# Kernel optimization log

Hardware: AMD Instinct MI355X
Metric: run time of the kernel (lower is better)

Reference implementation:

```python
import jax, jax.numpy as jnp
import numpy as np

DIM, HEADS, WH, WW, MLAT, MLON = 512, 8, 8, 8, 32, 64
N = WH * WW
B = MLAT * MLON
PER_LAT = (2 * WH - 1) * (2 * WW - 1)  # 225


def _make_rel_idx():
    # Swin 2D relative position index inside one window
    ch, cw = np.arange(WH), np.arange(WW)
    coords = np.stack(np.meshgrid(ch, cw, indexing='ij')).reshape(2, -1)  # (2, N)
    rel = coords[:, :, None] - coords[:, None, :]                          # (2, N, N)
    rel = rel.transpose(1, 2, 0).astype(np.int64)
    rel[..., 0] += WH - 1
    rel[..., 1] += WW - 1
    rel[..., 0] *= 2 * WW - 1
    idx2d = rel.sum(-1)                                                    # (N, N)
    # earth-specific: each lat row i gets its own 225-entry slab; lon diff is 0
    idx = idx2d[None] + np.arange(MLAT)[:, None, None] * PER_LAT           # (Mlat, N, N)
    idx = np.broadcast_to(idx[:, None], (MLAT, MLON, N, N)).reshape(B, N, N)
    return jnp.asarray(idx.astype(np.int32))


def setup_inputs() -> dict:
    key = jax.random.key(0)
    k = jax.random.split(key, 5)
    x = jax.random.normal(k[0], (B, N, DIM), dtype=jnp.float32)
    w_qkv = jax.random.normal(k[1], (3 * DIM, DIM), dtype=jnp.float32) * 0.02
    b_qkv = jnp.zeros((3 * DIM,), dtype=jnp.float32)
    w_proj = jax.random.normal(k[2], (DIM, DIM), dtype=jnp.float32) * 0.02
    b_proj = jnp.zeros((DIM,), dtype=jnp.float32)
    bias_table = jax.random.normal(k[3], (MLAT * PER_LAT, HEADS), dtype=jnp.float32) * 0.02
    return {
        'x': x, 'w_qkv': w_qkv, 'b_qkv': b_qkv,
        'w_proj': w_proj, 'b_proj': b_proj,
        'bias_table': bias_table, 'rel_idx': _make_rel_idx(),
    }


def reference(x, w_qkv, b_qkv, w_proj, b_proj, bias_table, rel_idx):
    Bn, Nn, C = x.shape
    D = C // HEADS
    qkv = (x @ w_qkv.T + b_qkv).reshape(Bn, Nn, 3, HEADS, D)
    q = jnp.transpose(qkv[:, :, 0], (0, 2, 1, 3))  # (B, H, N, D)
    k = jnp.transpose(qkv[:, :, 1], (0, 2, 1, 3))
    v = jnp.transpose(qkv[:, :, 2], (0, 2, 1, 3))
    # gather learned earth bias: (B, N, N, H) -> (B, H, N, N)
    bias = jnp.transpose(bias_table[rel_idx], (0, 3, 1, 2))
    scale = D ** -0.5  # SDPA default scale (qk_scale is None)
    attn = jax.nn.softmax(jnp.einsum('bhnd,bhmd->bhnm', q, k) * scale + bias, axis=-1)
    out = jnp.einsum('bhnm,bhmd->bhnd', attn, v)
    out = jnp.transpose(out, (0, 2, 1, 3)).reshape(Bn, Nn, C)
    return out @ w_proj.T + b_proj
```

## Files before the change

kernel.cpp:

```cpp
#include <hip/hip_runtime.h>
#include <stdint.h>

typedef __attribute__((ext_vector_type(8))) short short8;
typedef __attribute__((ext_vector_type(4))) short short4v;
typedef __attribute__((ext_vector_type(4))) float float4v;

__device__ __forceinline__ short f2bf(float f) {
  uint32_t u = __builtin_bit_cast(uint32_t, f);
  u += 0x7FFFu + ((u >> 16) & 1u);
  return (short)(u >> 16);
}

__device__ __forceinline__ void gl_lds16(const short* g, short* l) {
  __builtin_amdgcn_global_load_lds(
      (const __attribute__((address_space(1))) unsigned int*)g,
      (__attribute__((address_space(3))) unsigned int*)l, 16, 0, 0);
}

#define XPITCH 520
#define QPITCH 72

__global__ void prep_weights(const float* __restrict__ wq, const float* __restrict__ wp,
                             short* __restrict__ wq_b, short* __restrict__ wp_b) {
  int i = blockIdx.x * blockDim.x + threadIdx.x;
  int stride = gridDim.x * blockDim.x;
  for (int j = i; j < 786432 / 4; j += stride) {
    float4 v = ((const float4*)wq)[j];
    short4v t = {f2bf(v.x), f2bf(v.y), f2bf(v.z), f2bf(v.w)};
    ((short4v*)wq_b)[j] = t;
  }
  for (int j = i; j < 262144 / 4; j += stride) {
    float4 v = ((const float4*)wp)[j];
    short4v t = {f2bf(v.x), f2bf(v.y), f2bf(v.z), f2bf(v.w)};
    ((short4v*)wp_b)[j] = t;
  }
}

__global__ __launch_bounds__(512, 2)
void qkv_attn(const float* __restrict__ x, const short* __restrict__ wq,
              const float* __restrict__ bqkv, const float* __restrict__ btab,
              short* __restrict__ attn) {
  __shared__ short Xs[64 * XPITCH];
  __shared__ short Qs[2][64 * QPITCH];
  __shared__ short Ks[2][64 * QPITCH];
  __shared__ short Vt[2][64 * QPITCH];

  const int b    = blockIdx.x;
  const int tid  = threadIdx.x;
  const int lane = tid & 63;
  const int w    = tid >> 6;
  const int l16  = lane & 15;
  const int quad = lane >> 4;
  const int lat  = b >> 6;

  const float* xw = x + (size_t)b * (64 * 512);
  for (int c = tid; c < 64 * 128; c += 512) {
    int n = c >> 7, kc = c & 127;
    float4 v = *(const float4*)(xw + n * 512 + kc * 4);
    short4v t = {f2bf(v.x), f2bf(v.y), f2bf(v.z), f2bf(v.w)};
    *(short4v*)&Xs[n * XPITCH + kc * 4] = t;
  }
  __syncthreads();

  const int g  = w >> 2;
  const int st = w & 3;

  for (int h0 = 0; h0 < 8; h0 += 2) {
    {
      const int hq = h0 + g;
      const int hk = h0 + 1 - g;
      const short* Aq = wq + (size_t)((hq * 64 + st * 16 + l16) * 512) + quad * 8;
      const short* Ak = wq + (size_t)(((512) + hk * 64 + st * 16 + l16) * 512) + quad * 8;
      const short* Av = wq + (size_t)(((1024) + hq * 64 + st * 16 + l16) * 512) + quad * 8;
      const short* xb0 = &Xs[l16 * XPITCH + quad * 8];
      const short* xb1 = xb0 + 16 * XPITCH;
      const short* xb2 = xb0 + 32 * XPITCH;
      const short* xb3 = xb0 + 48 * XPITCH;

      float4v aQ[4] = {}, aK[4] = {}, aV[4] = {};
#pragma unroll 4
      for (int kk = 0; kk < 512; kk += 32) {
        short8 wqf = *(const short8*)(Aq + kk);
        short8 wkf = *(const short8*)(Ak + kk);
        short8 wvf = *(const short8*)(Av + kk);
        short8 x0 = *(const short8*)(xb0 + kk);
        short8 x1 = *(const short8*)(xb1 + kk);
        short8 x2 = *(const short8*)(xb2 + kk);
        short8 x3 = *(const short8*)(xb3 + kk);
        aQ[0] = __builtin_amdgcn_mfma_f32_16x16x32_bf16(wqf, x0, aQ[0], 0, 0, 0);
        aQ[1] = __builtin_amdgcn_mfma_f32_16x16x32_bf16(wqf, x1, aQ[1], 0, 0, 0);
        aQ[2] = __builtin_amdgcn_mfma_f32_16x16x32_bf16(wqf, x2, aQ[2], 0, 0, 0);
        aQ[3] = __builtin_amdgcn_mfma_f32_16x16x32_bf16(wqf, x3, aQ[3], 0, 0, 0);
        aK[0] = __builtin_amdgcn_mfma_f32_16x16x32_bf16(wkf, x0, aK[0], 0, 0, 0);
        aK[1] = __builtin_amdgcn_mfma_f32_16x16x32_bf16(wkf, x1, aK[1], 0, 0, 0);
        aK[2] = __builtin_amdgcn_mfma_f32_16x16x32_bf16(wkf, x2, aK[2], 0, 0, 0);
        aK[3] = __builtin_amdgcn_mfma_f32_16x16x32_bf16(wkf, x3, aK[3], 0, 0, 0);
        aV[0] = __builtin_amdgcn_mfma_f32_16x16x32_bf16(x0, wvf, aV[0], 0, 0, 0);
        aV[1] = __builtin_amdgcn_mfma_f32_16x16x32_bf16(x1, wvf, aV[1], 0, 0, 0);
        aV[2] = __builtin_amdgcn_mfma_f32_16x16x32_bf16(x2, wvf, aV[2], 0, 0, 0);
        aV[3] = __builtin_amdgcn_mfma_f32_16x16x32_bf16(x3, wvf, aV[3], 0, 0, 0);
      }

      float bq[4], bk[4];
#pragma unroll
      for (int i = 0; i < 4; ++i) {
        bq[i] = bqkv[hq * 64 + st * 16 + quad * 4 + i];
        bk[i] = bqkv[512 + hk * 64 + st * 16 + quad * 4 + i];
      }
      short* dq = &Qs[g][0];
      short* dk = &Ks[1 - g][0];
#pragma unroll
      for (int t = 0; t < 4; ++t) {
        int n = t * 16 + l16;
        short4v pq, pk;
#pragma unroll
        for (int i = 0; i < 4; ++i) {
          pq[i] = f2bf((aQ[t][i] + bq[i]) * 0.125f);
          pk[i] = f2bf(aK[t][i] + bk[i]);
        }
        *(short4v*)&dq[n * QPITCH + st * 16 + quad * 4] = pq;
        *(short4v*)&dk[n * QPITCH + st * 16 + quad * 4] = pk;
      }
      float bv = bqkv[1024 + hq * 64 + st * 16 + l16];
#pragma unroll
      for (int t = 0; t < 4; ++t) {
        short4v pv;
#pragma unroll
        for (int i = 0; i < 4; ++i) pv[i] = f2bf(aV[t][i] + bv);
        *(short4v*)&Vt[g][(st * 16 + l16) * QPITCH + t * 16 + quad * 4] = pv;
      }
    }
    __syncthreads();

    {
      const int hsel = w >> 2;
      const int h    = h0 + hsel;
      const int n0   = (w & 3) * 16;

      float4v s4[4] = {};
#pragma unroll
      for (int kd = 0; kd < 64; kd += 32) {
        short8 a = *(const short8*)&Qs[hsel][(n0 + l16) * QPITCH + kd + quad * 8];
#pragma unroll
        for (int t = 0; t < 4; ++t) {
          short8 bf = *(const short8*)&Ks[hsel][(t * 16 + l16) * QPITCH + kd + quad * 8];
          s4[t] = __builtin_amdgcn_mfma_f32_16x16x32_bf16(a, bf, s4[t], 0, 0, 0);
        }
      }
#pragma unroll
      for (int t = 0; t < 4; ++t) {
        int m = t * 16 + l16;
#pragma unroll
        for (int i = 0; i < 4; ++i) {
          int n = n0 + quad * 4 + i;
          int idx = ((n >> 3) - (m >> 3) + 7) * 15 + ((n & 7) - (m & 7) + 7) + lat * 225;
          s4[t][i] += btab[idx * 8 + h];
        }
      }
      float p[4][4];
#pragma unroll
      for (int i = 0; i < 4; ++i) {
        float mx = fmaxf(fmaxf(s4[0][i], s4[1][i]), fmaxf(s4[2][i], s4[3][i]));
        mx = fmaxf(mx, __shfl_xor(mx, 1));
        mx = fmaxf(mx, __shfl_xor(mx, 2));
        mx = fmaxf(mx, __shfl_xor(mx, 4));
        mx = fmaxf(mx, __shfl_xor(mx, 8));
        float e0 = __expf(s4[0][i] - mx), e1 = __expf(s4[1][i] - mx);
        float e2 = __expf(s4[2][i] - mx), e3 = __expf(s4[3][i] - mx);
        float sm = e0 + e1 + e2 + e3;
        sm += __shfl_xor(sm, 1);
        sm += __shfl_xor(sm, 2);
        sm += __shfl_xor(sm, 4);
        sm += __shfl_xor(sm, 8);
        float inv = 1.0f / sm;
        p[0][i] = e0 * inv; p[1][i] = e1 * inv; p[2][i] = e2 * inv; p[3][i] = e3 * inv;
      }
#pragma unroll
      for (int t = 0; t < 4; ++t)
#pragma unroll
        for (int i = 0; i < 4; ++i)
          Qs[hsel][(n0 + quad * 4 + i) * QPITCH + t * 16 + l16] = f2bf(p[t][i]);

      float4v o4[4] = {};
#pragma unroll
      for (int km = 0; km < 64; km += 32) {
        short8 a = *(const short8*)&Qs[hsel][(n0 + l16) * QPITCH + km + quad * 8];
#pragma unroll
        for (int t = 0; t < 4; ++t) {
          short8 bf = *(const short8*)&Vt[hsel][(t * 16 + l16) * QPITCH + km + quad * 8];
          o4[t] = __builtin_amdgcn_mfma_f32_16x16x32_bf16(a, bf, o4[t], 0, 0, 0);
        }
      }
      short* ob = attn + (size_t)b * (64 * 512);
#pragma unroll
      for (int t = 0; t < 4; ++t)
#pragma unroll
        for (int i = 0; i < 4; ++i)
          ob[(n0 + quad * 4 + i) * 512 + h * 64 + t * 16 + l16] = f2bf(o4[t][i]);
    }
    __syncthreads();
  }
}

__global__ __launch_bounds__(256, 2)
void proj_gemm(const short* __restrict__ attn, const short* __restrict__ wp,
               const float* __restrict__ bproj, float* __restrict__ out) {
  __shared__ short As[128 * 64];
  __shared__ short Bs[128 * 64];

  const int orig = blockIdx.x;
  const int wg   = (orig & 7) * 512 + (orig >> 3);
  const int n0   = (wg & 3) * 128;
  const int m0   = (wg >> 2) * 128;

  const int tid  = threadIdx.x;
  const int lane = tid & 63;
  const int w    = tid >> 6;
  const int l16  = lane & 15;
  const int quad = lane >> 4;
  const int wm   = w >> 1, wn = w & 1;

  const int srow = lane >> 3;
  const int scol = (lane & 7) * 8;

  float4v acc[4][4] = {};

  for (int kk = 0; kk < 512; kk += 64) {
#pragma unroll
    for (int j = 0; j < 4; ++j) {
      int chunk = w * 4 + j;
      int row = chunk * 8 + srow;
      gl_lds16(attn + (size_t)(m0 + row) * 512 + kk + scol, &As[chunk * 512]);
      gl_lds16(wp + (size_t)(n0 + row) * 512 + kk + scol, &Bs[chunk * 512]);
    }
    __syncthreads();
#pragma unroll
    for (int ks = 0; ks < 64; ks += 32) {
      short8 a[4], bf[4];
#pragma unroll
      for (int ti = 0; ti < 4; ++ti)
        a[ti] = *(const short8*)&As[(wm * 64 + ti * 16 + l16) * 64 + ks + quad * 8];
#pragma unroll
      for (int tj = 0; tj < 4; ++tj)
        bf[tj] = *(const short8*)&Bs[(wn * 64 + tj * 16 + l16) * 64 + ks + quad * 8];
#pragma unroll
      for (int ti = 0; ti < 4; ++ti)
#pragma unroll
        for (int tj = 0; tj < 4; ++tj)
          acc[ti][tj] = __builtin_amdgcn_mfma_f32_16x16x32_bf16(a[ti], bf[tj], acc[ti][tj], 0, 0, 0);
    }
    __syncthreads();
  }

  float bj[4];
#pragma unroll
  for (int tj = 0; tj < 4; ++tj) bj[tj] = bproj[n0 + wn * 64 + tj * 16 + l16];
#pragma unroll
  for (int ti = 0; ti < 4; ++ti)
#pragma unroll
    for (int i = 0; i < 4; ++i) {
      size_t rowoff = (size_t)(m0 + wm * 64 + ti * 16 + quad * 4 + i) * 512;
#pragma unroll
      for (int tj = 0; tj < 4; ++tj)
        out[rowoff + n0 + wn * 64 + tj * 16 + l16] = acc[ti][tj][i] + bj[tj];
    }
}

extern "C" void kernel_launch(void* const* d_in, const int* in_sizes, int n_in,
                              void* d_out, int out_size, void* d_ws, size_t ws_size,
                              hipStream_t stream) {
  const float* x     = (const float*)d_in[0];
  const float* wqkv  = (const float*)d_in[1];
  const float* bqkv  = (const float*)d_in[2];
  const float* wproj = (const float*)d_in[3];
  const float* bproj = (const float*)d_in[4];
  const float* btab  = (const float*)d_in[5];
  float* out = (float*)d_out;

  short* wq_b = (short*)d_ws;
  short* wp_b = wq_b + 786432;
  short* attn = wp_b + 262144;

  prep_weights<<<256, 256, 0, stream>>>(wqkv, wproj, wq_b, wp_b);
  qkv_attn<<<2048, 512, 0, stream>>>(x, wq_b, bqkv, btab, attn);
  proj_gemm<<<4096, 256, 0, stream>>>(attn, wp_b, bproj, out);
}
```

Baseline: 1.063 ms.

## Swizzle LDS layouts, process four heads per block, double-buffer projection GEMM

The padded LDS pitches are replaced by XOR-swizzled layouts for the X, Q, K, V and P tiles in the attention kernel and for the projection GEMM tiles. This is meant to avoid bank conflicts without wasting LDS on padding. The attention kernel now runs 1024 threads per block and handles four heads per pass instead of two, halving the number of head-loop iterations and barriers. The projection GEMM moves to 512 threads with smaller per-wave tiles and a two-stage LDS double buffer, so global-to-LDS loads overlap MFMA work. In exchange, LDS use per block grows to the full budget and register pressure is tighter under the new launch bounds.

```diff
diff --git a/kernel.cpp b/kernel.cpp
--- a/kernel.cpp
+++ b/kernel.cpp
@@ -17,8 +17,6 @@
       (__attribute__((address_space(3))) unsigned int*)l, 16, 0, 0);
 }
 
-#define XPITCH 520
-#define QPITCH 72
 
 __global__ void prep_weights(const float* __restrict__ wq, const float* __restrict__ wp,
                              short* __restrict__ wq_b, short* __restrict__ wp_b) {
@@ -36,14 +34,14 @@
   }
 }
 
-__global__ __launch_bounds__(512, 2)
+__global__ __launch_bounds__(1024, 4)
 void qkv_attn(const float* __restrict__ x, const short* __restrict__ wq,
               const float* __restrict__ bqkv, const float* __restrict__ btab,
               short* __restrict__ attn) {
-  __shared__ short Xs[64 * XPITCH];
-  __shared__ short Qs[2][64 * QPITCH];
-  __shared__ short Ks[2][64 * QPITCH];
-  __shared__ short Vt[2][64 * QPITCH];
+  __shared__ short Xs[64 * 512];
+  __shared__ short Qs[4][64 * 64];
+  __shared__ short Ks[4][64 * 64];
+  __shared__ short Vt[4][64 * 64];
 
   const int b    = blockIdx.x;
   const int tid  = threadIdx.x;
@@ -52,41 +50,45 @@
   const int l16  = lane & 15;
   const int quad = lane >> 4;
   const int lat  = b >> 6;
+  const int r    = l16 & 7;
+  const int offE = ((quad ^ (r & 3)) << 3) | ((r >> 2) << 5);
+  const int offO = offE ^ 32;
 
   const float* xw = x + (size_t)b * (64 * 512);
-  for (int c = tid; c < 64 * 128; c += 512) {
+  for (int c = tid; c < 64 * 128; c += 1024) {
     int n = c >> 7, kc = c & 127;
     float4 v = *(const float4*)(xw + n * 512 + kc * 4);
     short4v t = {f2bf(v.x), f2bf(v.y), f2bf(v.z), f2bf(v.w)};
-    *(short4v*)&Xs[n * XPITCH + kc * 4] = t;
+    *(short4v*)&Xs[n * 512 + ((kc * 4) ^ ((n & 7) << 3))] = t;
   }
   __syncthreads();
 
   const int g  = w >> 2;
   const int st = w & 3;
 
-  for (int h0 = 0; h0 < 8; h0 += 2) {
+#pragma unroll 1
+  for (int h0 = 0; h0 < 8; h0 += 4) {
     {
       const int hq = h0 + g;
-      const int hk = h0 + 1 - g;
+      const int hk = h0 + (g ^ 1);
       const short* Aq = wq + (size_t)((hq * 64 + st * 16 + l16) * 512) + quad * 8;
-      const short* Ak = wq + (size_t)(((512) + hk * 64 + st * 16 + l16) * 512) + quad * 8;
-      const short* Av = wq + (size_t)(((1024) + hq * 64 + st * 16 + l16) * 512) + quad * 8;
-      const short* xb0 = &Xs[l16 * XPITCH + quad * 8];
-      const short* xb1 = xb0 + 16 * XPITCH;
-      const short* xb2 = xb0 + 32 * XPITCH;
-      const short* xb3 = xb0 + 48 * XPITCH;
+      const short* Ak = wq + (size_t)((512 + hk * 64 + st * 16 + l16) * 512) + quad * 8;
+      const short* Av = wq + (size_t)((1024 + hq * 64 + st * 16 + l16) * 512) + quad * 8;
+      const short* xE = &Xs[l16 * 512 + offE];
+      const short* xO = &Xs[l16 * 512 + offO];
 
       float4v aQ[4] = {}, aK[4] = {}, aV[4] = {};
-#pragma unroll 4
-      for (int kk = 0; kk < 512; kk += 32) {
-        short8 wqf = *(const short8*)(Aq + kk);
-        short8 wkf = *(const short8*)(Ak + kk);
-        short8 wvf = *(const short8*)(Av + kk);
-        short8 x0 = *(const short8*)(xb0 + kk);
-        short8 x1 = *(const short8*)(xb1 + kk);
-        short8 x2 = *(const short8*)(xb2 + kk);
-        short8 x3 = *(const short8*)(xb3 + kk);
+#pragma unroll
+      for (int j = 0; j < 16; ++j) {
+        const short* xb = (j & 1) ? xO : xE;
+        const int xoff = (j >> 1) * 64;
+        short8 wqf = *(const short8*)(Aq + j * 32);
+        short8 wkf = *(const short8*)(Ak + j * 32);
+        short8 wvf = *(const short8*)(Av + j * 32);
+        short8 x0 = *(const short8*)(xb + xoff);
+        short8 x1 = *(const short8*)(xb + 8192 + xoff);
+        short8 x2 = *(const short8*)(xb + 16384 + xoff);
+        short8 x3 = *(const short8*)(xb + 24576 + xoff);
         aQ[0] = __builtin_amdgcn_mfma_f32_16x16x32_bf16(wqf, x0, aQ[0], 0, 0, 0);
         aQ[1] = __builtin_amdgcn_mfma_f32_16x16x32_bf16(wqf, x1, aQ[1], 0, 0, 0);
         aQ[2] = __builtin_amdgcn_mfma_f32_16x16x32_bf16(wqf, x2, aQ[2], 0, 0, 0);
@@ -108,7 +110,8 @@
         bk[i] = bqkv[512 + hk * 64 + st * 16 + quad * 4 + i];
       }
       short* dq = &Qs[g][0];
-      short* dk = &Ks[1 - g][0];
+      short* dk = &Ks[g ^ 1][0];
+      const int swqk = (st * 16 + quad * 4) ^ (r << 3);
 #pragma unroll
       for (int t = 0; t < 4; ++t) {
         int n = t * 16 + l16;
@@ -118,16 +121,17 @@
           pq[i] = f2bf((aQ[t][i] + bq[i]) * 0.125f);
           pk[i] = f2bf(aK[t][i] + bk[i]);
         }
-        *(short4v*)&dq[n * QPITCH + st * 16 + quad * 4] = pq;
-        *(short4v*)&dk[n * QPITCH + st * 16 + quad * 4] = pk;
+        *(short4v*)&dq[n * 64 + swqk] = pq;
+        *(short4v*)&dk[n * 64 + swqk] = pk;
       }
       float bv = bqkv[1024 + hq * 64 + st * 16 + l16];
+      const int dv = st * 16 + l16;
 #pragma unroll
       for (int t = 0; t < 4; ++t) {
         short4v pv;
 #pragma unroll
         for (int i = 0; i < 4; ++i) pv[i] = f2bf(aV[t][i] + bv);
-        *(short4v*)&Vt[g][(st * 16 + l16) * QPITCH + t * 16 + quad * 4] = pv;
+        *(short4v*)&Vt[g][dv * 64 + ((t * 16 + quad * 4) ^ (r << 3))] = pv;
       }
     }
     __syncthreads();
@@ -136,14 +140,18 @@
       const int hsel = w >> 2;
       const int h    = h0 + hsel;
       const int n0   = (w & 3) * 16;
+      const short* Qb = &Qs[hsel][0];
+      const short* Kb = &Ks[hsel][0];
+      const short* Vb = &Vt[hsel][0];
 
       float4v s4[4] = {};
 #pragma unroll
-      for (int kd = 0; kd < 64; kd += 32) {
-        short8 a = *(const short8*)&Qs[hsel][(n0 + l16) * QPITCH + kd + quad * 8];
+      for (int j = 0; j < 2; ++j) {
+        const int o = j ? offO : offE;
+        short8 a = *(const short8*)&Qb[(n0 + l16) * 64 + o];
 #pragma unroll
         for (int t = 0; t < 4; ++t) {
-          short8 bf = *(const short8*)&Ks[hsel][(t * 16 + l16) * QPITCH + kd + quad * 8];
+          short8 bf = *(const short8*)&Kb[(t * 16 + l16) * 64 + o];
           s4[t] = __builtin_amdgcn_mfma_f32_16x16x32_bf16(a, bf, s4[t], 0, 0, 0);
         }
       }
@@ -175,19 +183,23 @@
         float inv = 1.0f / sm;
         p[0][i] = e0 * inv; p[1][i] = e1 * inv; p[2][i] = e2 * inv; p[3][i] = e3 * inv;
       }
+      short* Pw = &Qs[hsel][0];
 #pragma unroll
       for (int t = 0; t < 4; ++t)
 #pragma unroll
-        for (int i = 0; i < 4; ++i)
-          Qs[hsel][(n0 + quad * 4 + i) * QPITCH + t * 16 + l16] = f2bf(p[t][i]);
+        for (int i = 0; i < 4; ++i) {
+          int row = n0 + quad * 4 + i;
+          Pw[row * 64 + ((t * 16 + l16) ^ ((row & 7) << 3))] = f2bf(p[t][i]);
+        }
 
       float4v o4[4] = {};
 #pragma unroll
-      for (int km = 0; km < 64; km += 32) {
-        short8 a = *(const short8*)&Qs[hsel][(n0 + l16) * QPITCH + km + quad * 8];
+      for (int j = 0; j < 2; ++j) {
+        const int o = j ? offO : offE;
+        short8 a = *(const short8*)&Qb[(n0 + l16) * 64 + o];
 #pragma unroll
         for (int t = 0; t < 4; ++t) {
-          short8 bf = *(const short8*)&Vt[hsel][(t * 16 + l16) * QPITCH + km + quad * 8];
+          short8 bf = *(const short8*)&Vb[(t * 16 + l16) * 64 + o];
           o4[t] = __builtin_amdgcn_mfma_f32_16x16x32_bf16(a, bf, o4[t], 0, 0, 0);
         }
       }
@@ -202,11 +214,47 @@
   }
 }
 
-__global__ __launch_bounds__(256, 2)
+__device__ __forceinline__ void stage_tile(const short* __restrict__ ga,
+                                           const short* __restrict__ gb,
+                                           short* lA, short* lB,
+                                           int w, int srow, int scol) {
+#pragma unroll
+  for (int j = 0; j < 2; ++j) {
+    int c = w * 2 + j;
+    gl_lds16(ga + (size_t)(c * 8 + srow) * 512 + scol, &lA[c * 512]);
+    gl_lds16(gb + (size_t)(c * 8 + srow) * 512 + scol, &lB[c * 512]);
+  }
+}
+
+__device__ __forceinline__ void compute_tile(const short* As_, const short* Bs_,
+                                             float4v (&acc)[2][4],
+                                             int wm, int wn, int l16,
+                                             int offE, int offO) {
+#pragma unroll
+  for (int ks = 0; ks < 2; ++ks) {
+    const int o = ks ? offO : offE;
+    short8 a[2], bf[4];
+#pragma unroll
+    for (int ti = 0; ti < 2; ++ti)
+      a[ti] = *(const short8*)&As_[(wm * 32 + ti * 16 + l16) * 64 + o];
+#pragma unroll
+    for (int tj = 0; tj < 4; ++tj)
+      bf[tj] = *(const short8*)&Bs_[(wn * 64 + tj * 16 + l16) * 64 + o];
+#pragma unroll
+    for (int ti = 0; ti < 2; ++ti)
+#pragma unroll
+      for (int tj = 0; tj < 4; ++tj)
+        acc[ti][tj] = __builtin_amdgcn_mfma_f32_16x16x32_bf16(a[ti], bf[tj], acc[ti][tj], 0, 0, 0);
+  }
+}
+
+__global__ __launch_bounds__(512, 4)
 void proj_gemm(const short* __restrict__ attn, const short* __restrict__ wp,
                const float* __restrict__ bproj, float* __restrict__ out) {
-  __shared__ short As[128 * 64];
-  __shared__ short Bs[128 * 64];
+  __shared__ short As0[128 * 64];
+  __shared__ short As1[128 * 64];
+  __shared__ short Bs0[128 * 64];
+  __shared__ short Bs1[128 * 64];
 
   const int orig = blockIdx.x;
   const int wg   = (orig & 7) * 512 + (orig >> 3);
@@ -219,36 +267,27 @@
   const int l16  = lane & 15;
   const int quad = lane >> 4;
   const int wm   = w >> 1, wn = w & 1;
+  const int r    = l16 & 7;
+  const int offE = ((quad ^ (r & 3)) << 3) | ((r >> 2) << 5);
+  const int offO = offE ^ 32;
 
   const int srow = lane >> 3;
-  const int scol = (lane & 7) * 8;
-
-  float4v acc[4][4] = {};
-
-  for (int kk = 0; kk < 512; kk += 64) {
-#pragma unroll
-    for (int j = 0; j < 4; ++j) {
-      int chunk = w * 4 + j;
-      int row = chunk * 8 + srow;
-      gl_lds16(attn + (size_t)(m0 + row) * 512 + kk + scol, &As[chunk * 512]);
-      gl_lds16(wp + (size_t)(n0 + row) * 512 + kk + scol, &Bs[chunk * 512]);
-    }
+  const int scol = ((lane & 7) ^ srow) * 8;
+
+  const short* gA = attn + (size_t)m0 * 512;
+  const short* gB = wp + (size_t)n0 * 512;
+
+  float4v acc[2][4] = {};
+
+  stage_tile(gA, gB, As0, Bs0, w, srow, scol);
+  __syncthreads();
+#pragma unroll
+  for (int kt = 0; kt < 8; kt += 2) {
+    if (kt + 1 < 8) stage_tile(gA + (kt + 1) * 64, gB + (kt + 1) * 64, As1, Bs1, w, srow, scol);
+    compute_tile(As0, Bs0, acc, wm, wn, l16, offE, offO);
     __syncthreads();
-#pragma unroll
-    for (int ks = 0; ks < 64; ks += 32) {
-      short8 a[4], bf[4];
-#pragma unroll
-      for (int ti = 0; ti < 4; ++ti)
-        a[ti] = *(const short8*)&As[(wm * 64 + ti * 16 + l16) * 64 + ks + quad * 8];
-#pragma unroll
-      for (int tj = 0; tj < 4; ++tj)
-        bf[tj] = *(const short8*)&Bs[(wn * 64 + tj * 16 + l16) * 64 + ks + quad * 8];
-#pragma unroll
-      for (int ti = 0; ti < 4; ++ti)
-#pragma unroll
-        for (int tj = 0; tj < 4; ++tj)
-          acc[ti][tj] = __builtin_amdgcn_mfma_f32_16x16x32_bf16(a[ti], bf[tj], acc[ti][tj], 0, 0, 0);
-    }
+    if (kt + 2 < 8) stage_tile(gA + (kt + 2) * 64, gB + (kt + 2) * 64, As0, Bs0, w, srow, scol);
+    compute_tile(As1, Bs1, acc, wm, wn, l16, offE, offO);
     __syncthreads();
   }
 
@@ -256,10 +295,10 @@
 #pragma unroll
   for (int tj = 0; tj < 4; ++tj) bj[tj] = bproj[n0 + wn * 64 + tj * 16 + l16];
 #pragma unroll
-  for (int ti = 0; ti < 4; ++ti)
+  for (int ti = 0; ti < 2; ++ti)
 #pragma unroll
     for (int i = 0; i < 4; ++i) {
-      size_t rowoff = (size_t)(m0 + wm * 64 + ti * 16 + quad * 4 + i) * 512;
+      size_t rowoff = (size_t)(m0 + wm * 32 + ti * 16 + quad * 4 + i) * 512;
 #pragma unroll
       for (int tj = 0; tj < 4; ++tj)
         out[rowoff + n0 + wn * 64 + tj * 16 + l16] = acc[ti][tj][i] + bj[tj];
@@ -282,6 +321,6 @@
   short* attn = wp_b + 262144;
 
   prep_weights<<<256, 256, 0, stream>>>(wqkv, wproj, wq_b, wp_b);
-  qkv_attn<<<2048, 512, 0, stream>>>(x, wq_b, bqkv, btab, attn);
-  proj_gemm<<<4096, 256, 0, stream>>>(attn, wp_b, bproj, out);
-}
+  qkv_attn<<<2048, 1024, 0, stream>>>(x, wq_b, bqkv, btab, attn);
+  proj_gemm<<<4096, 512, 0, stream>>>(attn, wp_b, bproj, out);
+}
```

New measurement: 1.069 ms. Within noise of the previous version (+0.5%).
